# Kernel optimization log

Measured on AMD Instinct MI355X. Metric: run time of the kernel, lower is better.

## Reference

```python
import jax, jax.numpy as jnp
import numpy as np

NUM_EMBEDDINGS = 8192
EMBEDDING_DIM = 64
COMMITMENT_COST = 0.25


def setup_inputs() -> dict:
    key = jax.random.key(0)
    kx, ke = jax.random.split(key)
    x = jax.random.normal(kx, (32, 1024, EMBEDDING_DIM), dtype=jnp.float32)
    embeddings = jax.random.normal(ke, (NUM_EMBEDDINGS, EMBEDDING_DIM), dtype=jnp.float32)
    return {"x": x, "embeddings": embeddings}


def reference(x, embeddings):
    d = embeddings.shape[1]
    flat_x = x.reshape(-1, d)  # [N, D]
    # squared euclidean distances (argmin identical to cdist argmin):
    d2 = (
        jnp.sum(flat_x * flat_x, axis=-1, keepdims=True)
        - 2.0 * flat_x @ embeddings.T
        + jnp.sum(embeddings * embeddings, axis=-1)
    )
    encoding_indices = jnp.argmin(d2, axis=1)  # [N]
    quantized = embeddings[encoding_indices].reshape(x.shape)
    codebook_loss = jnp.mean((jax.lax.stop_gradient(quantized) - x) ** 2)
    commitment_loss = COMMITMENT_COST * jnp.mean((quantized - jax.lax.stop_gradient(x)) ** 2)
    loss = codebook_loss + commitment_loss
    # straight-through estimator
    quantized_st = x + jax.lax.stop_gradient(quantized - x)
    return quantized_st, loss, encoding_indices
```

## Files before the change

### kernel.cpp

```cpp
#include <hip/hip_runtime.h>
#include <hip/hip_bf16.h>
#include <float.h>

#define N_ROWS 32768
#define DIMS   64
#define K_EMB  8192
#define NT     (K_EMB / 16)
#define NQ     8
#define NTQ    (NT / NQ)
#define RG     4
#define KEYMASK 0xFFFFFFC0u
#define GAP_THR 3.5e-3f

typedef __attribute__((ext_vector_type(8))) short s8v;
typedef __attribute__((ext_vector_type(4))) float f4v;
typedef __attribute__((ext_vector_type(4))) int   i4v;

#define WS_EFRAG 0
#define WS_EN2   (2 * 1024 * 1024)
#define WS_IDX   (WS_EN2 + K_EMB * 4)
#define WS_KEY   (WS_IDX + N_ROWS * 4)
#define WS_BH    (WS_KEY + N_ROWS * 8)
#define WS_SH    (WS_BH + NQ * N_ROWS * 4)
#define WS_CH    (WS_SH + NQ * N_ROWS * 4)
#define WS_CTL   (WS_CH + NQ * N_ROWS * 4)
#define WS_WL    (WS_CTL + 16)

#define OUT_LOSS (N_ROWS * DIMS)
#define OUT_IDX  (N_ROWS * DIMS + 1)

__device__ inline short bfh(float v) {
    __hip_bfloat16 h = __float2bfloat16(v);
    return __builtin_bit_cast(short, h);
}
__device__ inline float bff(short s) {
    __hip_bfloat16 h = __builtin_bit_cast(__hip_bfloat16, s);
    return __bfloat162float(h);
}

__global__ void vq_prep(const float* __restrict__ emb, short* __restrict__ efrag,
                        float* __restrict__ en2, int4* __restrict__ ctl) {
    if (blockIdx.x == 0 && threadIdx.x == 0) *ctl = make_int4(0, 0, 0, 0);
    int gid = blockIdx.x * 128 + threadIdx.x;
    int t = gid >> 6, lane = gid & 63;
    int m = lane & 15, q = lane >> 4;
    const float* er = emb + (size_t)(t * 16 + m) * DIMS;
    s8v hi0, lo0, hi1, lo1;
    float ss = 0.f;
#pragma unroll
    for (int j = 0; j < 8; ++j) {
        float v0 = er[q * 8 + j];
        float v1 = er[32 + q * 8 + j];
        ss += v0 * v0 + v1 * v1;
        short h0 = bfh(v0); lo0[j] = bfh(v0 - bff(h0)); hi0[j] = h0;
        short h1 = bfh(v1); lo1[j] = bfh(v1 - bff(h1)); hi1[j] = h1;
    }
    s8v* base = (s8v*)efrag + (size_t)t * 4 * 64;
    base[0 * 64 + lane] = hi0;
    base[1 * 64 + lane] = hi1;
    base[2 * 64 + lane] = lo0;
    base[3 * 64 + lane] = lo1;
    ss += __shfl_xor(ss, 16, 64);
    ss += __shfl_xor(ss, 32, 64);
    if (q == 0) en2[t * 16 + m] = -0.5f * ss;
}

#define LOADT(B0, B1, B2, B3, CC, T) do {                 \
    const i4v* _p = bsrc + (size_t)(T) * 256;             \
    B0 = _p[lane];       B1 = _p[64 + lane];              \
    B2 = _p[128 + lane]; B3 = _p[192 + lane];             \
    CC = ep[(T) * 16];                                    \
} while (0)

#define COMPT(B0, B1, B2, B3, CC, CODE) do {                                     \
    f4v cinit = {CC, CC, CC, CC};                 \
    _Pragma("unroll")                                                            \
    for (int g = 0; g < RG; ++g) {                                               \
        f4v acc;                                                                 \
        acc = __builtin_amdgcn_mfma_f32_16x16x32_bf16(ahi[g][0], __builtin_bit_cast(s8v, B0), cinit, 0, 0, 0); \
        acc = __builtin_amdgcn_mfma_f32_16x16x32_bf16(ahi[g][1], __builtin_bit_cast(s8v, B1), acc, 0, 0, 0);   \
        acc = __builtin_amdgcn_mfma_f32_16x16x32_bf16(ahi[g][0], __builtin_bit_cast(s8v, B2), acc, 0, 0, 0);   \
        acc = __builtin_amdgcn_mfma_f32_16x16x32_bf16(ahi[g][1], __builtin_bit_cast(s8v, B3), acc, 0, 0, 0);   \
        acc = __builtin_amdgcn_mfma_f32_16x16x32_bf16(alo[g][0], __builtin_bit_cast(s8v, B0), acc, 0, 0, 0);   \
        acc = __builtin_amdgcn_mfma_f32_16x16x32_bf16(alo[g][1], __builtin_bit_cast(s8v, B1), acc, 0, 0, 0);   \
        _Pragma("unroll")                                                        \
        for (int r = 0; r < 4; ++r) {        \
            float kf = __uint_as_float(                                          \
                (__float_as_uint(acc[r]) & KEYMASK) | (unsigned)(CODE));         \
            sec[g][r]  = __builtin_amdgcn_fmed3f(kf, sec[g][r], best[g][r]);     \
            best[g][r] = fmaxf(best[g][r], kf);                                  \
        }                                                                        \
    }                                                                            \
} while (0)

__global__ __launch_bounds__(64)
__attribute__((amdgpu_waves_per_eu(2, 3))) void vq_phase1(
    const float* __restrict__ x, const short* __restrict__ efrag,
    const float* __restrict__ en2,
    float* __restrict__ bh, float* __restrict__ sh, int* __restrict__ ch) {
    int lane = threadIdx.x;
    int m = lane & 15, q = lane >> 4;
    int kh = blockIdx.y;
    int row0 = blockIdx.x * 64;

    s8v ahi[RG][2], alo[RG][2];
#pragma unroll
    for (int g = 0; g < RG; ++g) {
        const float* xr = x + (size_t)(row0 + g * 16 + m) * DIMS + q * 8;
#pragma unroll
        for (int j = 0; j < 8; ++j) {
            float v0 = xr[j], v1 = xr[32 + j];
            short h0 = bfh(v0); alo[g][0][j] = bfh(v0 - bff(h0)); ahi[g][0][j] = h0;
            short h1 = bfh(v1); alo[g][1][j] = bfh(v1 - bff(h1)); ahi[g][1][j] = h1;
        }
    }

    float best[RG][4], sec[RG][4];
#pragma unroll
    for (int g = 0; g < RG; ++g)
#pragma unroll
        for (int r = 0; r < 4; ++r) { best[g][r] = -FLT_MAX; sec[g][r] = -FLT_MAX; }

    const i4v*   bsrc = (const i4v*)efrag + (size_t)kh * NTQ * 256;
    const float* ep   = en2 + (size_t)kh * NTQ * 16 + m;

    i4v A0, A1, A2, A3, B0, B1, B2, B3;
    float cA, cB;
    LOADT(A0, A1, A2, A3, cA, 0);
#pragma unroll 1
    for (int t = 0; t < NTQ; t += 2) {
        LOADT(B0, B1, B2, B3, cB, t + 1);
        COMPT(A0, A1, A2, A3, cA, t);
        if (t + 2 < NTQ) LOADT(A0, A1, A2, A3, cA, t + 2);
        COMPT(B0, B1, B2, B3, cB, t + 1);
    }

#pragma unroll
    for (int g = 0; g < RG; ++g)
#pragma unroll
    for (int r = 0; r < 4; ++r) {
        float b = best[g][r], sv = sec[g][r];
#pragma unroll
        for (int off = 1; off < 16; off <<= 1) {
            float ob = __shfl_xor(b, off, 64);
            float os = __shfl_xor(sv, off, 64);
            sv = fmaxf(fminf(b, ob), fmaxf(sv, os));
            b  = fmaxf(b, ob);
        }
        unsigned long long bal =
            __ballot(__float_as_uint(best[g][r]) == __float_as_uint(b));
        int win = __ffsll(bal >> (q * 16)) - 1;
        if (m == win) {
            int tl  = (int)(__float_as_uint(b) & 63u);
            int col = ((kh * NTQ + tl) << 4) | m;
            int o = kh * N_ROWS + row0 + g * 16 + q * 4 + r;
            bh[o] = b; sh[o] = sv; ch[o] = col;
        }
    }
}

__global__ void vq_merge(const float* __restrict__ bh, const float* __restrict__ sh,
                         const int* __restrict__ ch, int* __restrict__ idx_buf,
                         unsigned long long* __restrict__ key8,
                         float* __restrict__ nbv,
                         int* __restrict__ wl, int* __restrict__ wl_count) {
    int row = blockIdx.x * 256 + threadIdx.x;
    float nb = bh[row];
    int   c  = ch[row];
    float ns = -FLT_MAX;
#pragma unroll
    for (int h = 1; h < NQ; ++h) {
        float b = bh[h * N_ROWS + row];
        int   cc = ch[h * N_ROWS + row];
        if (b > nb) { ns = nb; nb = b; c = cc; }
        else        { ns = fmaxf(ns, b); }
    }
#pragma unroll
    for (int h = 0; h < NQ; ++h) ns = fmaxf(ns, sh[h * N_ROWS + row]);
    idx_buf[row] = c;
    key8[row] = 0ULL;
    nbv[row] = nb;
    if (nb - ns < GAP_THR) {
        int pos = atomicAdd(wl_count, 1);
        wl[pos] = row;
    }
}

__global__ __launch_bounds__(64) void vq_fixup(
    const float* __restrict__ x, const float* __restrict__ emb,
    const float* __restrict__ en2, const float* __restrict__ nbv,
    unsigned long long* __restrict__ key8,
    const int* __restrict__ wl, const int* __restrict__ wl_count) {
    int lane = threadIdx.x;
    int cchunk = blockIdx.x & 127;
    int rslice = blockIdx.x >> 7;
    int cnt = *wl_count;
    if (rslice >= cnt) return;
    int c = cchunk * 64 + lane;
    const float4* er = (const float4*)(emb + (size_t)c * DIMS);
    float4 e[16];
#pragma unroll
    for (int qq = 0; qq < 16; ++qq) e[qq] = er[qq];
    float c0 = en2[c];
    for (int wi = rslice; wi < cnt; wi += 16) {
        int row = wl[wi];
        const float4* xr = (const float4*)(x + (size_t)row * DIMS);
        float d = 0.f;
#pragma unroll
        for (int qq = 0; qq < 16; ++qq) {
            float4 ee = e[qq];
            float4 xx = xr[qq];
            d += ee.x * xx.x + ee.y * xx.y + ee.z * xx.z + ee.w * xx.w;
        }
        float bf_ = d + c0;
        int bc_ = c;
#pragma unroll
        for (int off = 1; off < 64; off <<= 1) {
            float of = __shfl_xor(bf_, off, 64);
            int   oc = __shfl_xor(bc_, off, 64);
            if (of > bf_ || (of == bf_ && oc < bc_)) { bf_ = of; bc_ = oc; }
        }
        if (lane == 0 && bf_ >= nbv[row] - GAP_THR) {
            unsigned int u = __float_as_uint(bf_);
            unsigned int sb = ((int)u < 0) ? ~u : (u | 0x80000000u);
            unsigned long long key = ((unsigned long long)sb << 32) | (unsigned int)(~bc_);
            atomicMax(&key8[row], key);
        }
    }
}

__global__ void vq_gather(const float* __restrict__ x, const float* __restrict__ emb,
                          const int* __restrict__ idx_buf,
                          const unsigned long long* __restrict__ key8,
                          float* __restrict__ out, double* __restrict__ loss_acc,
                          int* __restrict__ done_count) {
    int row = blockIdx.x * blockDim.x + threadIdx.x;
    unsigned long long k = key8[row];
    int idx = k ? (int)(~(unsigned int)k) : idx_buf[row];
    const float4* ev = (const float4*)(emb + (size_t)idx * DIMS);
    const float4* xv = (const float4*)(x + (size_t)row * DIMS);
    float4* ov = (float4*)(out + (size_t)row * DIMS);
    float s = 0.f;
#pragma unroll
    for (int qq = 0; qq < 16; ++qq) {
        float4 ee = ev[qq];
        float4 xx = xv[qq];
        float dx = ee.x - xx.x, dy = ee.y - xx.y, dz = ee.z - xx.z, dw = ee.w - xx.w;
        s += dx * dx + dy * dy + dz * dz + dw * dw;
        ov[qq] = ee;
    }
#pragma unroll
    for (int off = 32; off > 0; off >>= 1) s += __shfl_down(s, off, 64);
    if ((threadIdx.x & 63) == 0) atomicAdd(loss_acc, (double)s);
    out[OUT_IDX + row] = (float)idx;
    __syncthreads();
    if (threadIdx.x == 0) {
        __threadfence();
        int d = atomicAdd(done_count, 1);
        if (d == (int)gridDim.x - 1) {
            double total = atomicAdd(loss_acc, 0.0);
            out[OUT_LOSS] = (float)(1.25 * total / (double)(N_ROWS * DIMS));
        }
    }
}

extern "C" void kernel_launch(void* const* d_in, const int* in_sizes, int n_in,
                              void* d_out, int out_size, void* d_ws, size_t ws_size,
                              hipStream_t stream) {
    const float* x   = (const float*)d_in[0];
    const float* emb = (const float*)d_in[1];
    float* out = (float*)d_out;
    char*  ws  = (char*)d_ws;

    short* efrag   = (short*)(ws + WS_EFRAG);
    float* en2     = (float*)(ws + WS_EN2);
    int*   idx_buf = (int*)(ws + WS_IDX);
    unsigned long long* key8 = (unsigned long long*)(ws + WS_KEY);
    float* bhb     = (float*)(ws + WS_BH);
    float* shb     = (float*)(ws + WS_SH);
    int*   chb     = (int*)(ws + WS_CH);
    double* loss_acc = (double*)(ws + WS_CTL);
    int*   wl_count  = (int*)(ws + WS_CTL + 8);
    int*   done_cnt  = (int*)(ws + WS_CTL + 12);
    int*   wl        = (int*)(ws + WS_WL);

    vq_prep<<<(NT * 64) / 128, 128, 0, stream>>>(emb, efrag, en2, (int4*)(ws + WS_CTL));
    vq_phase1<<<dim3(N_ROWS / 64, NQ), 64, 0, stream>>>(x, efrag, en2, bhb, shb, chb);
    vq_merge<<<N_ROWS / 256, 256, 0, stream>>>(bhb, shb, chb, idx_buf, key8, bhb, wl, wl_count);
    vq_fixup<<<2048, 64, 0, stream>>>(x, emb, en2, bhb, key8, wl, wl_count);
    vq_gather<<<N_ROWS / 256, 256, 0, stream>>>(x, emb, idx_buf, key8, out, loss_acc, done_cnt);
}
```

Measured before the change: 193.4 us.

## Fuse merge/fixup/gather into one persistent kernel with grid barriers; widen phase1 split

Replaces the three tail kernels (merge, fixup, gather) with one 512-block persistent kernel that separates the phases with a software grid barrier, removing two kernel launches and their gaps. Phase1 now splits the codebook into 16 parts instead of 8, which shrinks the tile-code bits in the key mask to 5. Its MFMA chain is interleaved across the four row groups to expose independent accumulators, and its occupancy bound is raised. The changes bring a spin-barrier that depends on all 512 blocks being co-resident, double the partial-result traffic into the merge, and slightly reduce key precision.

```diff
diff --git a/kernel.cpp b/kernel.cpp
--- a/kernel.cpp
+++ b/kernel.cpp
@@ -6,11 +6,12 @@
 #define DIMS   64
 #define K_EMB  8192
 #define NT     (K_EMB / 16)
-#define NQ     8
+#define NQ     16
 #define NTQ    (NT / NQ)
 #define RG     4
-#define KEYMASK 0xFFFFFFC0u
+#define KEYMASK 0xFFFFFFE0u
 #define GAP_THR 3.5e-3f
+#define TAILB 512
 
 typedef __attribute__((ext_vector_type(8))) short s8v;
 typedef __attribute__((ext_vector_type(4))) float f4v;
@@ -23,9 +24,9 @@
 #define WS_BH    (WS_KEY + N_ROWS * 8)
 #define WS_SH    (WS_BH + NQ * N_ROWS * 4)
 #define WS_CH    (WS_SH + NQ * N_ROWS * 4)
-#define WS_CTL   (WS_CH + NQ * N_ROWS * 4)
-#define WS_WL    (WS_CTL + 16)
-
+#define WS_NBV   (WS_CH + NQ * N_ROWS * 4)
+#define WS_CTL   (WS_NBV + N_ROWS * 4)
+#define WS_WL    (WS_CTL + 32)
 #define OUT_LOSS (N_ROWS * DIMS)
 #define OUT_IDX  (N_ROWS * DIMS + 1)
 
@@ -40,7 +41,7 @@
 
 __global__ void vq_prep(const float* __restrict__ emb, short* __restrict__ efrag,
                         float* __restrict__ en2, int4* __restrict__ ctl) {
-    if (blockIdx.x == 0 && threadIdx.x == 0) *ctl = make_int4(0, 0, 0, 0);
+    if (blockIdx.x == 0 && threadIdx.x == 0) { ctl[0] = make_int4(0,0,0,0); ctl[1] = make_int4(0,0,0,0); }
     int gid = blockIdx.x * 128 + threadIdx.x;
     int t = gid >> 6, lane = gid & 63;
     int m = lane & 15, q = lane >> 4;
@@ -72,29 +73,39 @@
     CC = ep[(T) * 16];                                    \
 } while (0)
 
+#define MF(AF, BB, CI) __builtin_amdgcn_mfma_f32_16x16x32_bf16(AF, __builtin_bit_cast(s8v, BB), CI, 0, 0, 0)
+
+#define KEYUP(AG, G, CODE) do {                                                  \
+    _Pragma("unroll")                                                            \
+    for (int r = 0; r < 4; ++r) {            \
+        float kf = __uint_as_float(                                              \
+            (__float_as_uint(AG[r]) & KEYMASK) | (unsigned)(CODE));              \
+        sec[G][r]  = __builtin_amdgcn_fmed3f(kf, sec[G][r], best[G][r]);         \
+        best[G][r] = fmaxf(best[G][r], kf);                                      \
+    }                                                                            \
+} while (0)
+
 #define COMPT(B0, B1, B2, B3, CC, CODE) do {                                     \
     f4v cinit = {CC, CC, CC, CC};                 \
-    _Pragma("unroll")                                                            \
-    for (int g = 0; g < RG; ++g) {                                               \
-        f4v acc;                                                                 \
-        acc = __builtin_amdgcn_mfma_f32_16x16x32_bf16(ahi[g][0], __builtin_bit_cast(s8v, B0), cinit, 0, 0, 0); \
-        acc = __builtin_amdgcn_mfma_f32_16x16x32_bf16(ahi[g][1], __builtin_bit_cast(s8v, B1), acc, 0, 0, 0);   \
-        acc = __builtin_amdgcn_mfma_f32_16x16x32_bf16(ahi[g][0], __builtin_bit_cast(s8v, B2), acc, 0, 0, 0);   \
-        acc = __builtin_amdgcn_mfma_f32_16x16x32_bf16(ahi[g][1], __builtin_bit_cast(s8v, B3), acc, 0, 0, 0);   \
-        acc = __builtin_amdgcn_mfma_f32_16x16x32_bf16(alo[g][0], __builtin_bit_cast(s8v, B0), acc, 0, 0, 0);   \
-        acc = __builtin_amdgcn_mfma_f32_16x16x32_bf16(alo[g][1], __builtin_bit_cast(s8v, B1), acc, 0, 0, 0);   \
-        _Pragma("unroll")                                                        \
-        for (int r = 0; r < 4; ++r) {        \
-            float kf = __uint_as_float(                                          \
-                (__float_as_uint(acc[r]) & KEYMASK) | (unsigned)(CODE));         \
-            sec[g][r]  = __builtin_amdgcn_fmed3f(kf, sec[g][r], best[g][r]);     \
-            best[g][r] = fmaxf(best[g][r], kf);                                  \
-        }                                                                        \
-    }                                                                            \
+    f4v a0, a1, a2, a3;                                                          \
+    a0 = MF(ahi[0][0], B0, cinit); a1 = MF(ahi[1][0], B0, cinit);                \
+    a2 = MF(ahi[2][0], B0, cinit); a3 = MF(ahi[3][0], B0, cinit);                \
+    a0 = MF(ahi[0][1], B1, a0); a1 = MF(ahi[1][1], B1, a1);                      \
+    a2 = MF(ahi[2][1], B1, a2); a3 = MF(ahi[3][1], B1, a3);                      \
+    a0 = MF(ahi[0][0], B2, a0); a1 = MF(ahi[1][0], B2, a1);                      \
+    a2 = MF(ahi[2][0], B2, a2); a3 = MF(ahi[3][0], B2, a3);                      \
+    a0 = MF(ahi[0][1], B3, a0); a1 = MF(ahi[1][1], B3, a1);                      \
+    a2 = MF(ahi[2][1], B3, a2); a3 = MF(ahi[3][1], B3, a3);                      \
+    a0 = MF(alo[0][0], B0, a0); a1 = MF(alo[1][0], B0, a1);                      \
+    a2 = MF(alo[2][0], B0, a2); a3 = MF(alo[3][0], B0, a3);                      \
+    a0 = MF(alo[0][1], B1, a0); a1 = MF(alo[1][1], B1, a1);                      \
+    a2 = MF(alo[2][1], B1, a2); a3 = MF(alo[3][1], B1, a3);                      \
+    KEYUP(a0, 0, CODE); KEYUP(a1, 1, CODE);                                      \
+    KEYUP(a2, 2, CODE); KEYUP(a3, 3, CODE);                                      \
 } while (0)
 
 __global__ __launch_bounds__(64)
-__attribute__((amdgpu_waves_per_eu(2, 3))) void vq_phase1(
+__attribute__((amdgpu_waves_per_eu(2, 5))) void vq_phase1(
     const float* __restrict__ x, const short* __restrict__ efrag,
     const float* __restrict__ en2,
     float* __restrict__ bh, float* __restrict__ sh, int* __restrict__ ch) {
@@ -151,7 +162,7 @@
             __ballot(__float_as_uint(best[g][r]) == __float_as_uint(b));
         int win = __ffsll(bal >> (q * 16)) - 1;
         if (m == win) {
-            int tl  = (int)(__float_as_uint(b) & 63u);
+            int tl  = (int)(__float_as_uint(b) & 31u);
             int col = ((kh * NTQ + tl) << 4) | m;
             int o = kh * N_ROWS + row0 + g * 16 + q * 4 + r;
             bh[o] = b; sh[o] = sv; ch[o] = col;
@@ -159,108 +170,134 @@
     }
 }
 
-__global__ void vq_merge(const float* __restrict__ bh, const float* __restrict__ sh,
-                         const int* __restrict__ ch, int* __restrict__ idx_buf,
-                         unsigned long long* __restrict__ key8,
-                         float* __restrict__ nbv,
-                         int* __restrict__ wl, int* __restrict__ wl_count) {
-    int row = blockIdx.x * 256 + threadIdx.x;
-    float nb = bh[row];
-    int   c  = ch[row];
-    float ns = -FLT_MAX;
-#pragma unroll
-    for (int h = 1; h < NQ; ++h) {
-        float b = bh[h * N_ROWS + row];
-        int   cc = ch[h * N_ROWS + row];
-        if (b > nb) { ns = nb; nb = b; c = cc; }
-        else        { ns = fmaxf(ns, b); }
-    }
-#pragma unroll
-    for (int h = 0; h < NQ; ++h) ns = fmaxf(ns, sh[h * N_ROWS + row]);
-    idx_buf[row] = c;
-    key8[row] = 0ULL;
-    nbv[row] = nb;
-    if (nb - ns < GAP_THR) {
-        int pos = atomicAdd(wl_count, 1);
-        wl[pos] = row;
-    }
-}
-
-__global__ __launch_bounds__(64) void vq_fixup(
-    const float* __restrict__ x, const float* __restrict__ emb,
-    const float* __restrict__ en2, const float* __restrict__ nbv,
-    unsigned long long* __restrict__ key8,
-    const int* __restrict__ wl, const int* __restrict__ wl_count) {
-    int lane = threadIdx.x;
-    int cchunk = blockIdx.x & 127;
-    int rslice = blockIdx.x >> 7;
-    int cnt = *wl_count;
-    if (rslice >= cnt) return;
-    int c = cchunk * 64 + lane;
-    const float4* er = (const float4*)(emb + (size_t)c * DIMS);
-    float4 e[16];
-#pragma unroll
-    for (int qq = 0; qq < 16; ++qq) e[qq] = er[qq];
-    float c0 = en2[c];
-    for (int wi = rslice; wi < cnt; wi += 16) {
-        int row = wl[wi];
-        const float4* xr = (const float4*)(x + (size_t)row * DIMS);
-        float d = 0.f;
-#pragma unroll
-        for (int qq = 0; qq < 16; ++qq) {
-            float4 ee = e[qq];
-            float4 xx = xr[qq];
-            d += ee.x * xx.x + ee.y * xx.y + ee.z * xx.z + ee.w * xx.w;
-        }
-        float bf_ = d + c0;
-        int bc_ = c;
-#pragma unroll
-        for (int off = 1; off < 64; off <<= 1) {
-            float of = __shfl_xor(bf_, off, 64);
-            int   oc = __shfl_xor(bc_, off, 64);
-            if (of > bf_ || (of == bf_ && oc < bc_)) { bf_ = of; bc_ = oc; }
-        }
-        if (lane == 0 && bf_ >= nbv[row] - GAP_THR) {
-            unsigned int u = __float_as_uint(bf_);
-            unsigned int sb = ((int)u < 0) ? ~u : (u | 0x80000000u);
-            unsigned long long key = ((unsigned long long)sb << 32) | (unsigned int)(~bc_);
-            atomicMax(&key8[row], key);
-        }
-    }
-}
-
-__global__ void vq_gather(const float* __restrict__ x, const float* __restrict__ emb,
-                          const int* __restrict__ idx_buf,
-                          const unsigned long long* __restrict__ key8,
-                          float* __restrict__ out, double* __restrict__ loss_acc,
-                          int* __restrict__ done_count) {
-    int row = blockIdx.x * blockDim.x + threadIdx.x;
-    unsigned long long k = key8[row];
-    int idx = k ? (int)(~(unsigned int)k) : idx_buf[row];
-    const float4* ev = (const float4*)(emb + (size_t)idx * DIMS);
-    const float4* xv = (const float4*)(x + (size_t)row * DIMS);
-    float4* ov = (float4*)(out + (size_t)row * DIMS);
-    float s = 0.f;
-#pragma unroll
-    for (int qq = 0; qq < 16; ++qq) {
-        float4 ee = ev[qq];
-        float4 xx = xv[qq];
-        float dx = ee.x - xx.x, dy = ee.y - xx.y, dz = ee.z - xx.z, dw = ee.w - xx.w;
-        s += dx * dx + dy * dy + dz * dz + dw * dw;
-        ov[qq] = ee;
-    }
-#pragma unroll
-    for (int off = 32; off > 0; off >>= 1) s += __shfl_down(s, off, 64);
-    if ((threadIdx.x & 63) == 0) atomicAdd(loss_acc, (double)s);
-    out[OUT_IDX + row] = (float)idx;
+__device__ inline void gridsync(int* bar, int* gen) {
     __syncthreads();
     if (threadIdx.x == 0) {
-        __threadfence();
-        int d = atomicAdd(done_count, 1);
-        if (d == (int)gridDim.x - 1) {
-            double total = atomicAdd(loss_acc, 0.0);
-            out[OUT_LOSS] = (float)(1.25 * total / (double)(N_ROWS * DIMS));
-        }
+        int g = __hip_atomic_load(gen, __ATOMIC_RELAXED, __HIP_MEMORY_SCOPE_AGENT);
+        int a = __hip_atomic_fetch_add(bar, 1, __ATOMIC_ACQ_REL, __HIP_MEMORY_SCOPE_AGENT);
+        if (a == TAILB - 1) {
+            __hip_atomic_store(bar, 0, __ATOMIC_RELAXED, __HIP_MEMORY_SCOPE_AGENT);
+            __hip_atomic_fetch_add(gen, 1, __ATOMIC_RELEASE, __HIP_MEMORY_SCOPE_AGENT);
+        } else {
+            while (__hip_atomic_load(gen, __ATOMIC_ACQUIRE, __HIP_MEMORY_SCOPE_AGENT) <= g)
+                __builtin_amdgcn_s_sleep(2);
+        }
+    }
+    __syncthreads();
+}
+
+__global__ __launch_bounds__(256) void vq_tail(
+    const float* __restrict__ x, const float* __restrict__ emb,
+    const float* __restrict__ en2,
+    const float* __restrict__ bh, const float* __restrict__ sh,
+    const int* __restrict__ ch,
+    int* __restrict__ idx_buf, unsigned long long* __restrict__ key8,
+    float* __restrict__ nbv, int* __restrict__ wl, int* __restrict__ wl_count,
+    float* __restrict__ out, double* __restrict__ loss_acc,
+    int* __restrict__ bar, int* __restrict__ gen) {
+    int tid = threadIdx.x, bid = blockIdx.x;
+    int lane = tid & 63;
+
+    if (tid < 64) {
+        int row = bid * 64 + tid;
+        float nb = bh[row];
+        int   c  = ch[row];
+        float ns = -FLT_MAX;
+#pragma unroll
+        for (int h = 1; h < NQ; ++h) {
+            float b = bh[h * N_ROWS + row];
+            int   cc = ch[h * N_ROWS + row];
+            if (b > nb) { ns = nb; nb = b; c = cc; }
+            else        { ns = fmaxf(ns, b); }
+        }
+#pragma unroll
+        for (int h = 0; h < NQ; ++h) ns = fmaxf(ns, sh[h * N_ROWS + row]);
+        idx_buf[row] = c;
+        key8[row] = 0ULL;
+        nbv[row] = nb;
+        if (nb - ns < GAP_THR) {
+            int pos = atomicAdd(wl_count, 1);
+            wl[pos] = row;
+        }
+    }
+    gridsync(bar, gen);
+
+    {
+        int cnt;
+        if (lane == 0) cnt = __hip_atomic_load(wl_count, __ATOMIC_RELAXED, __HIP_MEMORY_SCOPE_AGENT);
+        cnt = __shfl(cnt, 0, 64);
+        int wwid = bid * 4 + (tid >> 6);
+        int cchunk = wwid & 127;
+        int rslice = wwid >> 7;
+        if (rslice < cnt) {
+            int c = cchunk * 64 + lane;
+            const float4* er = (const float4*)(emb + (size_t)c * DIMS);
+            float4 e[16];
+#pragma unroll
+            for (int qq = 0; qq < 16; ++qq) e[qq] = er[qq];
+            float c0 = en2[c];
+            for (int wi = rslice; wi < cnt; wi += 16) {
+                int row;
+                if (lane == 0) row = __hip_atomic_load(&wl[wi], __ATOMIC_RELAXED, __HIP_MEMORY_SCOPE_AGENT);
+                row = __shfl(row, 0, 64);
+                const float4* xr = (const float4*)(x + (size_t)row * DIMS);
+                float d = 0.f;
+#pragma unroll
+                for (int qq = 0; qq < 16; ++qq) {
+                    float4 ee = e[qq];
+                    float4 xx = xr[qq];
+                    d += ee.x * xx.x + ee.y * xx.y + ee.z * xx.z + ee.w * xx.w;
+                }
+                float bf_ = d + c0;
+                int bc_ = c;
+#pragma unroll
+                for (int off = 1; off < 64; off <<= 1) {
+                    float of = __shfl_xor(bf_, off, 64);
+                    int   oc = __shfl_xor(bc_, off, 64);
+                    if (of > bf_ || (of == bf_ && oc < bc_)) { bf_ = of; bc_ = oc; }
+                }
+                if (lane == 0) {
+                    float nb = __hip_atomic_load(&nbv[row], __ATOMIC_RELAXED, __HIP_MEMORY_SCOPE_AGENT);
+                    if (bf_ >= nb - GAP_THR) {
+                        unsigned int u = __float_as_uint(bf_);
+                        unsigned int sb = ((int)u < 0) ? ~u : (u | 0x80000000u);
+                        unsigned long long key = ((unsigned long long)sb << 32) | (unsigned int)(~bc_);
+                        atomicMax(&key8[row], key);
+                    }
+                }
+            }
+        }
+    }
+    gridsync(bar, gen);
+
+    {
+        int row = bid * 64 + (tid >> 2), part = tid & 3;
+        unsigned long long k = 0ULL;
+        if (part == 0) k = __hip_atomic_load(&key8[row], __ATOMIC_RELAXED, __HIP_MEMORY_SCOPE_AGENT);
+        k = __shfl(k, lane & ~3, 64);
+        int idx = k ? (int)(~(unsigned int)k) : idx_buf[row];
+        const float4* ev = (const float4*)(emb + (size_t)idx * DIMS);
+        const float4* xv = (const float4*)(x + (size_t)row * DIMS);
+        float4* ov = (float4*)(out + (size_t)row * DIMS);
+        float s = 0.f;
+#pragma unroll
+        for (int j = 0; j < 4; ++j) {
+            int qq = part * 4 + j;
+            float4 ee = ev[qq];
+            float4 xx = xv[qq];
+            float dx = ee.x - xx.x, dy = ee.y - xx.y, dz = ee.z - xx.z, dw = ee.w - xx.w;
+            s += dx * dx + dy * dy + dz * dz + dw * dw;
+            ov[qq] = ee;
+        }
+#pragma unroll
+        for (int off = 1; off < 64; off <<= 1) s += __shfl_xor(s, off, 64);
+        if (lane == 0) atomicAdd(loss_acc, (double)s);
+        if (part == 0) out[OUT_IDX + row] = (float)idx;
+    }
+    gridsync(bar, gen);
+    if (bid == 0 && tid == 0) {
+        double total = atomicAdd(loss_acc, 0.0);
+        out[OUT_LOSS] = (float)(1.25 * total / (double)(N_ROWS * DIMS));
     }
 }
 
@@ -279,14 +316,15 @@
     float* bhb     = (float*)(ws + WS_BH);
     float* shb     = (float*)(ws + WS_SH);
     int*   chb     = (int*)(ws + WS_CH);
+    float* nbv     = (float*)(ws + WS_NBV);
     double* loss_acc = (double*)(ws + WS_CTL);
     int*   wl_count  = (int*)(ws + WS_CTL + 8);
-    int*   done_cnt  = (int*)(ws + WS_CTL + 12);
+    int*   bar       = (int*)(ws + WS_CTL + 16);
+    int*   gen       = (int*)(ws + WS_CTL + 20);
     int*   wl        = (int*)(ws + WS_WL);
 
     vq_prep<<<(NT * 64) / 128, 128, 0, stream>>>(emb, efrag, en2, (int4*)(ws + WS_CTL));
     vq_phase1<<<dim3(N_ROWS / 64, NQ), 64, 0, stream>>>(x, efrag, en2, bhb, shb, chb);
-    vq_merge<<<N_ROWS / 256, 256, 0, stream>>>(bhb, shb, chb, idx_buf, key8, bhb, wl, wl_count);
-    vq_fixup<<<2048, 64, 0, stream>>>(x, emb, en2, bhb, key8, wl, wl_count);
-    vq_gather<<<N_ROWS / 256, 256, 0, stream>>>(x, emb, idx_buf, key8, out, loss_acc, done_cnt);
-}
+    vq_tail<<<TAILB, 256, 0, stream>>>(x, emb, en2, bhb, shb, chb, idx_buf, key8, nbv,
+                                       wl, wl_count, out, loss_acc, bar, gen);
+}
```

After: 413.6 us. 114% more time.
